# Optimization experiments

Measured on AMD Instinct MI355X. Metric: run time of the kernel, lower is better.

The kernel has to match this reference:

```python
import jax, jax.numpy as jnp
import numpy as np
import math

B, S, D, H = 2, 2048, 1024, 16
DK = D // H
THETA = 10000.0

def _rope_tables(seq_len, dk, theta):
    freqs = 1.0 / theta ** (np.arange(0, dk, 2)[: dk // 2].astype(np.float32) / dk)
    t = np.arange(seq_len, dtype=np.float32)
    ang = np.outer(t, freqs)  # [S, dk/2]
    return jnp.asarray(np.cos(ang)), jnp.asarray(np.sin(ang))

def setup_inputs() -> dict:
    key = jax.random.key(0)
    ks = jax.random.split(key, 12)
    init = lambda k, shape: (0.02 * jax.random.normal(k, shape)).astype(jnp.float32)
    cos, sin = _rope_tables(S, DK, THETA)
    mask = jnp.tril(jnp.ones((S, S), dtype=jnp.int32))[None, None]  # [1,1,S,S] causal
    return {
        'Q': jax.random.normal(ks[0], (B, S, D), jnp.float32),
        'K': jax.random.normal(ks[1], (B, S, D), jnp.float32),
        'V': jax.random.normal(ks[2], (B, S, D), jnp.float32),
        'mask': mask,
        'Wq_w': init(ks[3], (D, D)), 'Wq_b': init(ks[4], (D,)),
        'Wk_w': init(ks[5], (D, D)), 'Wk_b': init(ks[6], (D,)),
        'Wv_w': init(ks[7], (D, D)), 'Wv_b': init(ks[8], (D,)),
        'Wo_w': init(ks[9], (D, D)), 'Wo_b': init(ks[10], (D,)),
        'cos': cos, 'sin': sin,
    }

def _apply_rope(x, cos, sin):
    # x: [B, S, H, DK]; cos/sin: [S, DK/2]
    x1 = x[..., 0::2]
    x2 = x[..., 1::2]
    c = cos[None, :, None, :]
    s = sin[None, :, None, :]
    out_even = x1 * c - x2 * s
    out_odd = x1 * s + x2 * c
    return jnp.stack([out_even, out_odd], axis=-1).reshape(x.shape)

def reference(Q, K, V, mask, Wq_w, Wq_b, Wk_w, Wk_b, Wv_w, Wv_b, Wo_w, Wo_b, cos, sin):
    b, s, d = Q.shape
    q = (Q @ Wq_w.T + Wq_b).reshape(b, s, H, DK)
    k = (K @ Wk_w.T + Wk_b).reshape(b, s, H, DK)
    v = (V @ Wv_w.T + Wv_b).reshape(b, s, H, DK)
    q = _apply_rope(q, cos[:s], sin[:s])
    k = _apply_rope(k, cos[:s], sin[:s])
    # [B,H,S,DK]
    q = q.transpose(0, 2, 1, 3)
    k = k.transpose(0, 2, 1, 3)
    v = v.transpose(0, 2, 1, 3)
    scores = jnp.einsum('bhqd,bhkd->bhqk', q, k) / math.sqrt(DK)
    scores = jnp.where(mask == 0, jnp.float32(-1e9), scores)
    probs = jax.nn.softmax(scores, axis=-1)
    out = jnp.einsum('bhqk,bhkd->bhqd', probs, v)  # [B,H,S,DK]
    out = out.transpose(0, 2, 1, 3).reshape(b, s, d)
    return out @ Wo_w.T + Wo_b
```

## Files before the change

### kernel.cpp

```cpp
#include <hip/hip_runtime.h>
#include <cstdint>
#include <cstddef>


typedef __bf16 bf16x8 __attribute__((ext_vector_type(8)));
typedef float floatx4 __attribute__((ext_vector_type(4)));

#define DI __device__ __forceinline__

DI unsigned short f2bf(float f) {
  union { float f; unsigned int u; } v; v.f = f;
  unsigned int r = v.u + 0x7fffu + ((v.u >> 16) & 1u);
  return (unsigned short)(r >> 16);
}

DI unsigned short bfb(float f) {
  __bf16 h = (__bf16)f;
  union { __bf16 h; unsigned short u; } c; c.h = h;
  return c.u;
}

DI void async_ld16(const void* g, void* l) {
  __builtin_amdgcn_global_load_lds(
      (const __attribute__((address_space(1))) unsigned int*)g,
      (__attribute__((address_space(3))) unsigned int*)l, 16, 0, 0);
}

__global__ void cvt_all(const float* __restrict__ Q, const float* __restrict__ K,
                        const float* __restrict__ V, const float* __restrict__ Wq,
                        const float* __restrict__ Wk, const float* __restrict__ Wv,
                        const float* __restrict__ Wo, unsigned short* __restrict__ dst) {
  int i = blockIdx.x * blockDim.x + threadIdx.x;
  const float* s;
  int off;
  if (i < 3145728) {
    if (i < 1048576) { s = Q; off = i; }
    else if (i < 2097152) { s = K; off = i - 1048576; }
    else { s = V; off = i - 2097152; }
  } else {
    int j = i - 3145728;
    int wsel = j >> 18;
    off = j & 262143;
    s = (wsel == 0) ? Wq : (wsel == 1) ? Wk : (wsel == 2) ? Wv : Wo;
  }
  float4 f = reinterpret_cast<const float4*>(s)[off];
  ushort4 o;
  o.x = f2bf(f.x); o.y = f2bf(f.y); o.z = f2bf(f.z); o.w = f2bf(f.w);
  reinterpret_cast<ushort4*>(dst)[i] = o;
}

__global__ __launch_bounds__(256)
void gemm_qkv(const unsigned short* __restrict__ Qb, const unsigned short* __restrict__ Kb,
              const unsigned short* __restrict__ Vb, const unsigned short* __restrict__ Wq,
              const unsigned short* __restrict__ Wk, const unsigned short* __restrict__ Wv,
              const float* __restrict__ bq, const float* __restrict__ bk,
              const float* __restrict__ bv, unsigned short* __restrict__ qh,
              unsigned short* __restrict__ kh, unsigned short* __restrict__ vtp,
              const float* __restrict__ cosT, const float* __restrict__ sinT) {
  __shared__ unsigned short As[2][128 * 32];
  __shared__ unsigned short Bs[2][128 * 32];

  const int id = blockIdx.x;
  const int xb = id / 96;
  const int rem = id - xb * 96;
  const int proj = rem >> 5;
  const int yb = rem & 31;

  const unsigned short* X = (proj == 0) ? Qb : (proj == 1) ? Kb : Vb;
  const unsigned short* W = (proj == 0) ? Wq : (proj == 1) ? Wk : Wv;
  const float* bias = (proj == 0) ? bq : (proj == 1) ? bk : bv;
  unsigned short* outB = (proj == 0) ? qh : (proj == 1) ? kh : vtp;

  const int t = threadIdx.x;
  const int lane = t & 63;
  const int w = t >> 6;
  const int row0 = yb * 128;
  const int col0 = xb * 128;
  const int wm = (w >> 1) * 64;
  const int wn = (w & 1) * 64;
  const int fr = lane & 15;
  const int fk = (lane >> 4) * 8;
  const int rbase = (lane >> 4) * 4;

  floatx4 acc[4][4];
#pragma unroll
  for (int i = 0; i < 4; ++i)
#pragma unroll
    for (int j = 0; j < 4; ++j)
      acc[i][j] = (floatx4){0.f, 0.f, 0.f, 0.f};

  auto stage = [&](int k0, int buf) {
#pragma unroll
    for (int it = 0; it < 2; ++it) {
      int c = it * 256 + t;
      int r = c >> 2, cc = c & 3;
      async_ld16(X + (size_t)(row0 + r) * 1024 + k0 + cc * 8, &As[buf][c * 8]);
    }
#pragma unroll
    for (int it = 0; it < 2; ++it) {
      int c = it * 256 + t;
      int r = c >> 2, cc = c & 3;
      async_ld16(W + (size_t)(col0 + r) * 1024 + k0 + cc * 8, &Bs[buf][c * 8]);
    }
  };

  stage(0, 0);
  __syncthreads();

  for (int kb = 0; kb < 32; ++kb) {
    const int cur = kb & 1;
    if (kb + 1 < 32) stage((kb + 1) * 32, cur ^ 1);

    bf16x8 af[4], bfr[4];
#pragma unroll
    for (int i = 0; i < 4; ++i)
      af[i] = *reinterpret_cast<const bf16x8*>(&As[cur][(wm + i * 16 + fr) * 32 + fk]);
#pragma unroll
    for (int j = 0; j < 4; ++j)
      bfr[j] = *reinterpret_cast<const bf16x8*>(&Bs[cur][(wn + j * 16 + fr) * 32 + fk]);
    if (proj == 2) {
#pragma unroll
      for (int i = 0; i < 4; ++i)
#pragma unroll
        for (int j = 0; j < 4; ++j)
          acc[i][j] = __builtin_amdgcn_mfma_f32_16x16x32_bf16(bfr[j], af[i], acc[i][j], 0, 0, 0);
    } else {
#pragma unroll
      for (int i = 0; i < 4; ++i)
#pragma unroll
        for (int j = 0; j < 4; ++j)
          acc[i][j] = __builtin_amdgcn_mfma_f32_16x16x32_bf16(af[i], bfr[j], acc[i][j], 0, 0, 0);
    }
    __syncthreads();
  }

  if (proj < 2) {
#pragma unroll
    for (int j = 0; j < 4; ++j) {
      const int col = col0 + wn + j * 16 + fr;
      const float bvv = bias[col];
#pragma unroll
      for (int i = 0; i < 4; ++i) {
#pragma unroll
        for (int r = 0; r < 4; ++r) {
          const int row = row0 + wm + i * 16 + rbase + r;
          float v = acc[i][j][r] + bvv;
          const int bb = row >> 11, sp = row & 2047, hh = col >> 6, dk = col & 63;
          float p = __shfl_xor(v, 1);
          const int i2 = (col & 63) >> 1;
          const float cv = cosT[sp * 32 + i2];
          const float sv = sinT[sp * 32 + i2];
          float res = ((col & 1) == 0) ? (v * cv - p * sv) : (p * sv + v * cv);
          if (proj == 0) res *= 0.125f;
          outB[(((size_t)(bb * 16 + hh)) * 2048 + sp) * 64 + dk] = f2bf(res);
        }
      }
    }
  } else {
#pragma unroll
    for (int j = 0; j < 4; ++j) {
#pragma unroll
      for (int r = 0; r < 4; ++r) {
        const int dkc = col0 + wn + j * 16 + rbase + r;
        const float bvv = bias[dkc];
        const int hh = dkc >> 6, dk = dkc & 63;
#pragma unroll
        for (int i = 0; i < 4; ++i) {
          const int spf = row0 + wm + i * 16 + fr;
          const int bb = spf >> 11, sp = spf & 2047;
          vtp[(((size_t)(bb * 16 + hh)) * 64 + dk) * 2048 + sp] = f2bf(acc[i][j][r] + bvv);
        }
      }
    }
  }
}

__global__ __launch_bounds__(256)
void gemm_out(const unsigned short* __restrict__ X, const unsigned short* __restrict__ W,
              const float* __restrict__ bias, float* __restrict__ outF) {
  __shared__ unsigned short As[2][64 * 32];
  __shared__ unsigned short Bs[2][128 * 32];

  const int id = blockIdx.x;
  const int xb = id >> 6;
  const int yb = id & 63;

  const int t = threadIdx.x;
  const int lane = t & 63;
  const int w = t >> 6;
  const int row0 = yb * 64;
  const int col0 = xb * 128;
  const int wm = (w >> 1) * 32;
  const int wn = (w & 1) * 64;
  const int fr = lane & 15;
  const int fk = (lane >> 4) * 8;
  const int rbase = (lane >> 4) * 4;

  floatx4 acc[2][4];
#pragma unroll
  for (int i = 0; i < 2; ++i)
#pragma unroll
    for (int j = 0; j < 4; ++j)
      acc[i][j] = (floatx4){0.f, 0.f, 0.f, 0.f};

  auto stage = [&](int k0, int buf) {
    {
      int c = t;
      int r = c >> 2, cc = c & 3;
      async_ld16(X + (size_t)(row0 + r) * 1024 + k0 + cc * 8, &As[buf][c * 8]);
    }
#pragma unroll
    for (int it = 0; it < 2; ++it) {
      int c = it * 256 + t;
      int r = c >> 2, cc = c & 3;
      async_ld16(W + (size_t)(col0 + r) * 1024 + k0 + cc * 8, &Bs[buf][c * 8]);
    }
  };

  stage(0, 0);
  __syncthreads();

  for (int kb = 0; kb < 32; ++kb) {
    const int cur = kb & 1;
    if (kb + 1 < 32) stage((kb + 1) * 32, cur ^ 1);

    bf16x8 af[2], bfr[4];
#pragma unroll
    for (int i = 0; i < 2; ++i)
      af[i] = *reinterpret_cast<const bf16x8*>(&As[cur][(wm + i * 16 + fr) * 32 + fk]);
#pragma unroll
    for (int j = 0; j < 4; ++j)
      bfr[j] = *reinterpret_cast<const bf16x8*>(&Bs[cur][(wn + j * 16 + fr) * 32 + fk]);
#pragma unroll
    for (int i = 0; i < 2; ++i)
#pragma unroll
      for (int j = 0; j < 4; ++j)
        acc[i][j] = __builtin_amdgcn_mfma_f32_16x16x32_bf16(af[i], bfr[j], acc[i][j], 0, 0, 0);
    __syncthreads();
  }

#pragma unroll
  for (int j = 0; j < 4; ++j) {
    const int col = col0 + wn + j * 16 + fr;
    const float bvv = bias[col];
#pragma unroll
    for (int i = 0; i < 2; ++i)
#pragma unroll
      for (int r = 0; r < 4; ++r) {
        const int row = row0 + wm + i * 16 + rbase + r;
        outF[(size_t)row * 1024 + col] = acc[i][j][r] + bvv;
      }
  }
}

__global__ __launch_bounds__(256)
void flash_attn(const unsigned short* __restrict__ qh,
                const unsigned short* __restrict__ kh,
                const unsigned short* __restrict__ vt,
                unsigned short* __restrict__ out) {
  __shared__ unsigned short Ks[2][64 * 64];
  __shared__ unsigned short Vs[2][64 * 64];
  __shared__ unsigned short Ps[8][16 * 64];

  const int t = threadIdx.x, lane = t & 63, w = t >> 6;
  const int g = lane >> 4;
  const int fr = lane & 15;
  const int fk = g * 8;
  const int rbase = g * 4;
  const int id = blockIdx.x;
  const int qbA = id >> 5;
  const int bh = id & 31;
  const int qbB = 31 - qbA;
  const int qwA = qbA * 64 + w * 16;
  const int qwB = qbB * 64 + w * 16;

  const size_t baseQK = (size_t)bh * 2048 * 64;
  const size_t baseV = (size_t)bh * 64 * 2048;

  bf16x8 qfA[2], qfB[2];
  qfA[0] = *reinterpret_cast<const bf16x8*>(&qh[baseQK + (size_t)(qwA + fr) * 64 + fk]);
  qfA[1] = *reinterpret_cast<const bf16x8*>(&qh[baseQK + (size_t)(qwA + fr) * 64 + 32 + fk]);
  qfB[0] = *reinterpret_cast<const bf16x8*>(&qh[baseQK + (size_t)(qwB + fr) * 64 + fk]);
  qfB[1] = *reinterpret_cast<const bf16x8*>(&qh[baseQK + (size_t)(qwB + fr) * 64 + 32 + fk]);

  floatx4 oA[4], oB[4];
  float lA[4], lB[4];
#pragma unroll
  for (int i = 0; i < 4; ++i) {
    oA[i] = (floatx4){0.f, 0.f, 0.f, 0.f};
    oB[i] = (floatx4){0.f, 0.f, 0.f, 0.f};
    lA[i] = 0.f; lB[i] = 0.f;
  }

  auto stage = [&](int kb, int buf) {
    const int k0 = kb * 64;
#pragma unroll
    for (int it = 0; it < 2; ++it) {
      int c = it * 256 + t;
      int r = c >> 3, cg = (c & 7) ^ (r & 7);
      async_ld16(kh + baseQK + (size_t)(k0 + r) * 64 + cg * 8, &Ks[buf][c * 8]);
    }
#pragma unroll
    for (int it = 0; it < 2; ++it) {
      int c = it * 256 + t;
      int r = c >> 3, cg = (c & 7) ^ (r & 7);
      async_ld16(vt + baseV + (size_t)r * 2048 + k0 + cg * 8, &Vs[buf][c * 8]);
    }
  };

  const int nkb = qbB + 1;
  stage(0, 0);
  __syncthreads();

  for (int kb = 0; kb < nkb; ++kb) {
    const int cur = kb & 1;
    if (kb + 1 < nkb) stage(kb + 1, cur ^ 1);
    const int k0 = kb * 64;
    const bool aAct = (kb <= qbA);

    bf16x8 kf[4][2];
#pragma unroll
    for (int j = 0; j < 4; ++j)
#pragma unroll
      for (int kk = 0; kk < 2; ++kk)
        kf[j][kk] = *reinterpret_cast<const bf16x8*>(
            &Ks[cur][(j * 16 + fr) * 64 + ((((kk << 2) | g) ^ (fr & 7)) << 3)]);

    floatx4 sB[4], sA[4];
#pragma unroll
    for (int j = 0; j < 4; ++j) {
      sB[j] = (floatx4){0.f, 0.f, 0.f, 0.f};
      sA[j] = (floatx4){0.f, 0.f, 0.f, 0.f};
    }
#pragma unroll
    for (int j = 0; j < 4; ++j)
#pragma unroll
      for (int kk = 0; kk < 2; ++kk)
        sB[j] = __builtin_amdgcn_mfma_f32_16x16x32_bf16(qfB[kk], kf[j][kk], sB[j], 0, 0, 0);
    if (aAct) {
#pragma unroll
      for (int j = 0; j < 4; ++j)
#pragma unroll
        for (int kk = 0; kk < 2; ++kk)
          sA[j] = __builtin_amdgcn_mfma_f32_16x16x32_bf16(qfA[kk], kf[j][kk], sA[j], 0, 0, 0);
    }

    if (k0 + 63 > qwB) {
#pragma unroll
      for (int j = 0; j < 4; ++j)
#pragma unroll
        for (int r = 0; r < 4; ++r)
          if (k0 + j * 16 + fr > qwB + rbase + r) sB[j][r] = -1e30f;
    }
    if (aAct && k0 + 63 > qwA) {
#pragma unroll
      for (int j = 0; j < 4; ++j)
#pragma unroll
        for (int r = 0; r < 4; ++r)
          if (k0 + j * 16 + fr > qwA + rbase + r) sA[j][r] = -1e30f;
    }

#pragma unroll
    for (int j = 0; j < 4; ++j) {
      const int chb = (j * 16 + fr) >> 3;
      const int cin = fr & 7;
#pragma unroll
      for (int r = 0; r < 4; ++r) {
        const int row = rbase + r;
        float pB = __expf(sB[j][r]);
        lB[r] += pB;
        Ps[w][row * 64 + ((chb ^ (row & 7)) << 3) + cin] = bfb(pB);
      }
    }
    if (aAct) {
#pragma unroll
      for (int j = 0; j < 4; ++j) {
        const int chb = (j * 16 + fr) >> 3;
        const int cin = fr & 7;
#pragma unroll
        for (int r = 0; r < 4; ++r) {
          const int row = rbase + r;
          float pA = __expf(sA[j][r]);
          lA[r] += pA;
          Ps[w + 4][row * 64 + ((chb ^ (row & 7)) << 3) + cin] = bfb(pA);
        }
      }
    }

    bf16x8 vf[4][2], pB2[2], pA2[2];
#pragma unroll
    for (int id2 = 0; id2 < 4; ++id2)
#pragma unroll
      for (int kk = 0; kk < 2; ++kk)
        vf[id2][kk] = *reinterpret_cast<const bf16x8*>(
            &Vs[cur][(id2 * 16 + fr) * 64 + ((((kk << 2) | g) ^ (fr & 7)) << 3)]);
#pragma unroll
    for (int kk = 0; kk < 2; ++kk)
      pB2[kk] = *reinterpret_cast<const bf16x8*>(
          &Ps[w][fr * 64 + ((((kk << 2) | g) ^ (fr & 7)) << 3)]);
#pragma unroll
    for (int kk = 0; kk < 2; ++kk)
#pragma unroll
      for (int id2 = 0; id2 < 4; ++id2)
        oB[id2] = __builtin_amdgcn_mfma_f32_16x16x32_bf16(pB2[kk], vf[id2][kk], oB[id2], 0, 0, 0);
    if (aAct) {
#pragma unroll
      for (int kk = 0; kk < 2; ++kk)
        pA2[kk] = *reinterpret_cast<const bf16x8*>(
            &Ps[w + 4][fr * 64 + ((((kk << 2) | g) ^ (fr & 7)) << 3)]);
#pragma unroll
      for (int kk = 0; kk < 2; ++kk)
#pragma unroll
        for (int id2 = 0; id2 < 4; ++id2)
          oA[id2] = __builtin_amdgcn_mfma_f32_16x16x32_bf16(pA2[kk], vf[id2][kk], oA[id2], 0, 0, 0);
    }

    __syncthreads();
  }

#pragma unroll
  for (int r = 0; r < 4; ++r) {
#pragma unroll
    for (int d = 1; d < 16; d <<= 1) {
      lB[r] += __shfl_xor(lB[r], d);
      lA[r] += __shfl_xor(lA[r], d);
    }
  }

  const int bb = bh >> 4, hh = bh & 15;
#pragma unroll
  for (int id2 = 0; id2 < 4; ++id2)
#pragma unroll
    for (int r = 0; r < 4; ++r) {
      const int qrA = qwA + rbase + r;
      const int qrB = qwB + rbase + r;
      out[((size_t)(bb * 2048 + qrA)) * 1024 + hh * 64 + id2 * 16 + fr] = bfb(oA[id2][r] / lA[r]);
      out[((size_t)(bb * 2048 + qrB)) * 1024 + hh * 64 + id2 * 16 + fr] = bfb(oB[id2][r] / lB[r]);
    }
}

extern "C" void kernel_launch(void* const* d_in, const int* in_sizes, int n_in,
                              void* d_out, int out_size, void* d_ws, size_t ws_size,
                              hipStream_t stream) {
  const float* Q  = (const float*)d_in[0];
  const float* K  = (const float*)d_in[1];
  const float* V  = (const float*)d_in[2];
  const float* Wq = (const float*)d_in[4];
  const float* bq = (const float*)d_in[5];
  const float* Wk = (const float*)d_in[6];
  const float* bk = (const float*)d_in[7];
  const float* Wv = (const float*)d_in[8];
  const float* bv = (const float*)d_in[9];
  const float* Wo = (const float*)d_in[10];
  const float* bo = (const float*)d_in[11];
  const float* cosT = (const float*)d_in[12];
  const float* sinT = (const float*)d_in[13];

  char* ws = (char*)d_ws;
  const size_t MB = 1024 * 1024;
  unsigned short* Qb  = (unsigned short*)(ws + 0 * MB);
  unsigned short* Kb  = (unsigned short*)(ws + 8 * MB);
  unsigned short* Vb  = (unsigned short*)(ws + 16 * MB);
  unsigned short* Wqb = (unsigned short*)(ws + 24 * MB);
  unsigned short* Wkb = (unsigned short*)(ws + 26 * MB);
  unsigned short* Wvb = (unsigned short*)(ws + 28 * MB);
  unsigned short* Wob = (unsigned short*)(ws + 30 * MB);
  unsigned short* qh  = (unsigned short*)(ws + 32 * MB);
  unsigned short* khp = (unsigned short*)(ws + 40 * MB);
  unsigned short* vtp = (unsigned short*)(ws + 48 * MB);
  unsigned short* ao  = (unsigned short*)(ws + 56 * MB);

  cvt_all<<<16384, 256, 0, stream>>>(Q, K, V, Wq, Wk, Wv, Wo, (unsigned short*)ws);

  gemm_qkv<<<768, 256, 0, stream>>>(Qb, Kb, Vb, Wqb, Wkb, Wvb, bq, bk, bv,
                                    qh, khp, vtp, cosT, sinT);
  flash_attn<<<512, 256, 0, stream>>>(qh, khp, vtp, ao);
  gemm_out<<<512, 256, 0, stream>>>(ao, Wob, bo, (float*)d_out);
}
```

Before: 260.3 us.

## Replace global_load_lds staging with register-prefetch then LDS store in all kernels

Swaps the direct global-to-LDS async loads for ordinary vectorized global loads into registers, issued before the compute of the current tile and written to the alternate LDS buffer after the MFMAs. The aim is to overlap global memory latency with MFMA work and avoid the waitcnt serialization that global_load_lds can force at the barrier. It costs extra VGPRs for the staging registers and adds explicit LDS write instructions, which may reduce occupancy. In the attention kernel the swizzle is now applied on the LDS destination instead of the global source.

```diff
diff --git a/kernel.cpp b/kernel.cpp
--- a/kernel.cpp
+++ b/kernel.cpp
@@ -18,12 +18,6 @@
   __bf16 h = (__bf16)f;
   union { __bf16 h; unsigned short u; } c; c.h = h;
   return c.u;
-}
-
-DI void async_ld16(const void* g, void* l) {
-  __builtin_amdgcn_global_load_lds(
-      (const __attribute__((address_space(1))) unsigned int*)g,
-      (__attribute__((address_space(3))) unsigned int*)l, 16, 0, 0);
 }
 
 __global__ void cvt_all(const float* __restrict__ Q, const float* __restrict__ K,
@@ -82,6 +76,12 @@
   const int fk = (lane >> 4) * 8;
   const int rbase = (lane >> 4) * 4;
 
+  const int c0 = t, c1 = t + 256;
+  const unsigned short* gA0 = X + (size_t)(row0 + (c0 >> 2)) * 1024 + (c0 & 3) * 8;
+  const unsigned short* gA1 = X + (size_t)(row0 + (c1 >> 2)) * 1024 + (c1 & 3) * 8;
+  const unsigned short* gB0 = W + (size_t)(col0 + (c0 >> 2)) * 1024 + (c0 & 3) * 8;
+  const unsigned short* gB1 = W + (size_t)(col0 + (c1 >> 2)) * 1024 + (c1 & 3) * 8;
+
   floatx4 acc[4][4];
 #pragma unroll
   for (int i = 0; i < 4; ++i)
@@ -89,27 +89,27 @@
     for (int j = 0; j < 4; ++j)
       acc[i][j] = (floatx4){0.f, 0.f, 0.f, 0.f};
 
-  auto stage = [&](int k0, int buf) {
-#pragma unroll
-    for (int it = 0; it < 2; ++it) {
-      int c = it * 256 + t;
-      int r = c >> 2, cc = c & 3;
-      async_ld16(X + (size_t)(row0 + r) * 1024 + k0 + cc * 8, &As[buf][c * 8]);
-    }
-#pragma unroll
-    for (int it = 0; it < 2; ++it) {
-      int c = it * 256 + t;
-      int r = c >> 2, cc = c & 3;
-      async_ld16(W + (size_t)(col0 + r) * 1024 + k0 + cc * 8, &Bs[buf][c * 8]);
-    }
-  };
-
-  stage(0, 0);
+  uint4 ra0, ra1, rb0, rb1;
+  auto gload = [&](int k0) {
+    ra0 = *reinterpret_cast<const uint4*>(gA0 + k0);
+    ra1 = *reinterpret_cast<const uint4*>(gA1 + k0);
+    rb0 = *reinterpret_cast<const uint4*>(gB0 + k0);
+    rb1 = *reinterpret_cast<const uint4*>(gB1 + k0);
+  };
+  auto swrite = [&](int buf) {
+    *reinterpret_cast<uint4*>(&As[buf][c0 * 8]) = ra0;
+    *reinterpret_cast<uint4*>(&As[buf][c1 * 8]) = ra1;
+    *reinterpret_cast<uint4*>(&Bs[buf][c0 * 8]) = rb0;
+    *reinterpret_cast<uint4*>(&Bs[buf][c1 * 8]) = rb1;
+  };
+
+  gload(0);
+  swrite(0);
   __syncthreads();
 
   for (int kb = 0; kb < 32; ++kb) {
     const int cur = kb & 1;
-    if (kb + 1 < 32) stage((kb + 1) * 32, cur ^ 1);
+    if (kb + 1 < 32) gload((kb + 1) * 32);
 
     bf16x8 af[4], bfr[4];
 #pragma unroll
@@ -131,6 +131,8 @@
         for (int j = 0; j < 4; ++j)
           acc[i][j] = __builtin_amdgcn_mfma_f32_16x16x32_bf16(af[i], bfr[j], acc[i][j], 0, 0, 0);
     }
+
+    if (kb + 1 < 32) swrite(cur ^ 1);
     __syncthreads();
   }
 
@@ -196,6 +198,11 @@
   const int fk = (lane >> 4) * 8;
   const int rbase = (lane >> 4) * 4;
 
+  const int c0 = t, c1 = t + 256;
+  const unsigned short* gA0 = X + (size_t)(row0 + (c0 >> 2)) * 1024 + (c0 & 3) * 8;
+  const unsigned short* gB0 = W + (size_t)(col0 + (c0 >> 2)) * 1024 + (c0 & 3) * 8;
+  const unsigned short* gB1 = W + (size_t)(col0 + (c1 >> 2)) * 1024 + (c1 & 3) * 8;
+
   floatx4 acc[2][4];
 #pragma unroll
   for (int i = 0; i < 2; ++i)
@@ -203,26 +210,25 @@
     for (int j = 0; j < 4; ++j)
       acc[i][j] = (floatx4){0.f, 0.f, 0.f, 0.f};
 
-  auto stage = [&](int k0, int buf) {
-    {
-      int c = t;
-      int r = c >> 2, cc = c & 3;
-      async_ld16(X + (size_t)(row0 + r) * 1024 + k0 + cc * 8, &As[buf][c * 8]);
-    }
-#pragma unroll
-    for (int it = 0; it < 2; ++it) {
-      int c = it * 256 + t;
-      int r = c >> 2, cc = c & 3;
-      async_ld16(W + (size_t)(col0 + r) * 1024 + k0 + cc * 8, &Bs[buf][c * 8]);
-    }
-  };
-
-  stage(0, 0);
+  uint4 ra0, rb0, rb1;
+  auto gload = [&](int k0) {
+    ra0 = *reinterpret_cast<const uint4*>(gA0 + k0);
+    rb0 = *reinterpret_cast<const uint4*>(gB0 + k0);
+    rb1 = *reinterpret_cast<const uint4*>(gB1 + k0);
+  };
+  auto swrite = [&](int buf) {
+    *reinterpret_cast<uint4*>(&As[buf][c0 * 8]) = ra0;
+    *reinterpret_cast<uint4*>(&Bs[buf][c0 * 8]) = rb0;
+    *reinterpret_cast<uint4*>(&Bs[buf][c1 * 8]) = rb1;
+  };
+
+  gload(0);
+  swrite(0);
   __syncthreads();
 
   for (int kb = 0; kb < 32; ++kb) {
     const int cur = kb & 1;
-    if (kb + 1 < 32) stage((kb + 1) * 32, cur ^ 1);
+    if (kb + 1 < 32) gload((kb + 1) * 32);
 
     bf16x8 af[2], bfr[4];
 #pragma unroll
@@ -236,6 +242,8 @@
 #pragma unroll
       for (int j = 0; j < 4; ++j)
         acc[i][j] = __builtin_amdgcn_mfma_f32_16x16x32_bf16(af[i], bfr[j], acc[i][j], 0, 0, 0);
+
+    if (kb + 1 < 32) swrite(cur ^ 1);
     __syncthreads();
   }
 
@@ -292,29 +300,33 @@
     lA[i] = 0.f; lB[i] = 0.f;
   }
 
-  auto stage = [&](int kb, int buf) {
+  const int sc0 = t, sc1 = t + 256;
+  const int r0 = sc0 >> 3, cc0 = sc0 & 7, d0 = (r0 * 8 + (cc0 ^ (r0 & 7))) * 8;
+  const int r1 = sc1 >> 3, cc1 = sc1 & 7, d1 = (r1 * 8 + (cc1 ^ (r1 & 7))) * 8;
+
+  uint4 rk0, rk1, rv0, rv1;
+  auto gload = [&](int kb) {
     const int k0 = kb * 64;
-#pragma unroll
-    for (int it = 0; it < 2; ++it) {
-      int c = it * 256 + t;
-      int r = c >> 3, cg = (c & 7) ^ (r & 7);
-      async_ld16(kh + baseQK + (size_t)(k0 + r) * 64 + cg * 8, &Ks[buf][c * 8]);
-    }
-#pragma unroll
-    for (int it = 0; it < 2; ++it) {
-      int c = it * 256 + t;
-      int r = c >> 3, cg = (c & 7) ^ (r & 7);
-      async_ld16(vt + baseV + (size_t)r * 2048 + k0 + cg * 8, &Vs[buf][c * 8]);
-    }
+    rk0 = *reinterpret_cast<const uint4*>(kh + baseQK + (size_t)(k0 + r0) * 64 + cc0 * 8);
+    rk1 = *reinterpret_cast<const uint4*>(kh + baseQK + (size_t)(k0 + r1) * 64 + cc1 * 8);
+    rv0 = *reinterpret_cast<const uint4*>(vt + baseV + (size_t)r0 * 2048 + k0 + cc0 * 8);
+    rv1 = *reinterpret_cast<const uint4*>(vt + baseV + (size_t)r1 * 2048 + k0 + cc1 * 8);
+  };
+  auto swrite = [&](int buf) {
+    *reinterpret_cast<uint4*>(&Ks[buf][d0]) = rk0;
+    *reinterpret_cast<uint4*>(&Ks[buf][d1]) = rk1;
+    *reinterpret_cast<uint4*>(&Vs[buf][d0]) = rv0;
+    *reinterpret_cast<uint4*>(&Vs[buf][d1]) = rv1;
   };
 
   const int nkb = qbB + 1;
-  stage(0, 0);
+  gload(0);
+  swrite(0);
   __syncthreads();
 
   for (int kb = 0; kb < nkb; ++kb) {
     const int cur = kb & 1;
-    if (kb + 1 < nkb) stage(kb + 1, cur ^ 1);
+    if (kb + 1 < nkb) gload(kb + 1);
     const int k0 = kb * 64;
     const bool aAct = (kb <= qbA);
 
@@ -415,6 +427,7 @@
           oA[id2] = __builtin_amdgcn_mfma_f32_16x16x32_bf16(pA2[kk], vf[id2][kk], oA[id2], 0, 0, 0);
     }
 
+    if (kb + 1 < nkb) swrite(cur ^ 1);
     __syncthreads();
   }
 
```

Result: faster. 249.0 us (-4.4%).
